# Kernel optimization log

Measured on AMD Instinct MI355X. Metric: run time of the kernel, lower is better.

The kernel has to match this reference:

```python
import jax, jax.numpy as jnp
import numpy as np

L, B, H, E, V = 64, 2048, 1024, 50, 256  # seq_len, batch, hidden, char_emb, char_vocab
PAD = 0


def setup_inputs() -> dict:
    key = jax.random.key(0)
    ks = jax.random.split(key, 10)
    s = 1.0 / np.sqrt(H)  # torch LSTM default init scale
    emb = jax.random.normal(ks[0], (V, E), jnp.float32)
    emb = emb.at[PAD].set(0.0)  # padding_idx row
    return {
        "input": jax.random.randint(ks[1], (L, B), 0, V, jnp.int32),
        "h0": jax.random.normal(ks[2], (1, B, H), jnp.float32),
        "c0": jax.random.normal(ks[3], (1, B, H), jnp.float32),
        "emb": emb,
        "W_ih": jax.random.uniform(ks[4], (4 * H, E), jnp.float32, -s, s),
        "W_hh": jax.random.uniform(ks[5], (4 * H, H), jnp.float32, -s, s),
        "b_ih": jax.random.uniform(ks[6], (4 * H,), jnp.float32, -s, s),
        "b_hh": jax.random.uniform(ks[7], (4 * H,), jnp.float32, -s, s),
        "W_proj": jax.random.uniform(ks[8], (V, H), jnp.float32, -s, s),
        "b_proj": jax.random.uniform(ks[9], (V,), jnp.float32, -s, s),
    }


def reference(input, h0, c0, emb, W_ih, W_hh, b_ih, b_hh, W_proj, b_proj):
    # char embedding lookup: (L, B, E)
    x = emb[input]
    b = b_ih + b_hh

    def step(carry, x_t):
        h, c = carry  # (B, H) each
        gates = x_t @ W_ih.T + h @ W_hh.T + b  # (B, 4H), torch gate order i,f,g,o
        i, f, g, o = jnp.split(gates, 4, axis=-1)
        c_new = jax.nn.sigmoid(f) * c + jax.nn.sigmoid(i) * jnp.tanh(g)
        h_new = jax.nn.sigmoid(o) * jnp.tanh(c_new)
        return (h_new, c_new), h_new

    (hT, cT), hs = jax.lax.scan(step, (h0[0], c0[0]), x)
    # per-step linear projection of hidden state (same math as looped Linear)
    scores = hs @ W_proj.T + b_proj  # (L, B, V)
    return scores, hT[None], cT[None]
```

## Files before the change

kernel.cpp:

```cpp
#include <hip/hip_runtime.h>
#include <hip/hip_bf16.h>
#include <cstdint>
#include <cstddef>

#define LSEQ  64
#define BATCH 2048
#define HID   1024
#define NGATE 4096
#define VOC   256
#define EMBD  50

using bf16 = __hip_bfloat16;
typedef __attribute__((ext_vector_type(8))) __bf16 bf16x8;
typedef __attribute__((ext_vector_type(4))) float  f32x4;

__device__ __forceinline__ void gload_lds16(const void* g, void* l) {
  __builtin_amdgcn_global_load_lds(
      (const __attribute__((address_space(1))) unsigned int*)g,
      (__attribute__((address_space(3))) unsigned int*)l, 16, 0, 0);
}

__device__ __forceinline__ float sigf(float x) {
  x = fminf(fmaxf(x, -30.f), 30.f);
  return 1.f / (1.f + __expf(-x));
}
__device__ __forceinline__ float tanh_f(float x) {
  x = fminf(fmaxf(x, -15.f), 15.f);
  float e = __expf(2.f * x);
  return (e - 1.f) / (e + 1.f);
}


__global__ void k_prep_whh(const float* __restrict__ W, bf16* __restrict__ Wr) {
  size_t i = (size_t)blockIdx.x * 256 + threadIdx.x;
  int k  = (int)(i & 1023);
  int np = (int)(i >> 10);
  int T = np >> 7, w = np & 127;
  int wc = w >> 6, g = (w >> 4) & 3, hl = w & 15;
  int grow = g * HID + T * 32 + wc * 16 + hl;
  Wr[i] = __float2bfloat16(W[(size_t)grow * HID + k]);
}

__global__ void k_prep_embw(const float* __restrict__ emb, const float* __restrict__ W_ih,
                            const float* __restrict__ b_ih, const float* __restrict__ b_hh,
                            float* __restrict__ embW) {
  size_t i = (size_t)blockIdx.x * 256 + threadIdx.x;
  int np = (int)(i & 4095);
  int v  = (int)(i >> 12);
  int T = np >> 7, w = np & 127;
  int wc = w >> 6, g = (w >> 4) & 3, hl = w & 15;
  int grow = g * HID + T * 32 + wc * 16 + hl;
  float s = b_ih[grow] + b_hh[grow];
  #pragma unroll 10
  for (int e = 0; e < EMBD; ++e)
    s += emb[(size_t)v * EMBD + e] * W_ih[(size_t)grow * EMBD + e];
  embW[i] = s;
}

__global__ void k_prep_wp(const float* __restrict__ Wp_f, bf16* __restrict__ Wp) {
  size_t i = (size_t)blockIdx.x * 256 + threadIdx.x;
  Wp[i] = __float2bfloat16(Wp_f[i]);
}

__global__ void k_init_state(const float* __restrict__ h0, const float* __restrict__ c0,
                             bf16* __restrict__ h, float* __restrict__ c) {
  size_t i = (size_t)blockIdx.x * 256 + threadIdx.x;
  h[i] = __float2bfloat16(h0[i]);
  c[i] = c0[i];
}

template<int MODE>
__global__ __launch_bounds__(512) void g8(
    const bf16* __restrict__ Abase, const bf16* __restrict__ Bbase,
    const float* __restrict__ c_in, float* __restrict__ c_out,
    bf16* __restrict__ h_out,
    const float* __restrict__ embW, const int* __restrict__ input,
    const float* __restrict__ b_proj, float* __restrict__ out,
    int t, int kc, int nslots)
{
  __shared__ __align__(16) bf16 lsA[4 * 256 * 32];
  __shared__ __align__(16) bf16 lsB[4 * 128 * 32];

  const int tid  = threadIdx.x;
  const int wave = tid >> 6, lane = tid & 63;
  const int wr = wave >> 1, wc = wave & 1;
  const int bx = blockIdx.x, by = blockIdx.y;

  const bf16* Asrc;
  if constexpr (MODE == 0) {
    Asrc = Abase + (size_t)bx * 256 * HID;
  } else {
    int t_local = bx >> 3;
    int slot = (kc + 1 + t_local) % nslots;
    Asrc = Abase + ((size_t)slot * BATCH + (size_t)(bx & 7) * 256) * HID;
  }
  const bf16* Bsrc = Bbase + (size_t)by * 128 * HID;

  const int srow = tid >> 2;
  const int xg   = (tid >> 3) & 3;
  const int colg = (((tid & 3) ^ xg) << 3);
  const bf16* pA0 = Asrc + (size_t)srow * HID + colg;
  const bf16* pA1 = Asrc + (size_t)(128 + srow) * HID + colg;
  const bf16* pB  = Bsrc + (size_t)srow * HID + colg;
  bf16* dA0 = lsA + wave * 512;
  bf16* dA1 = lsA + 4096 + wave * 512;
  bf16* dB  = lsB + wave * 512;

  const int hl = lane & 15;
  const int kk = (((lane >> 4) ^ ((lane >> 1) & 3)) << 3);
  int aofs[4], bofs[4];
  #pragma unroll
  for (int m = 0; m < 4; ++m) aofs[m] = (wr * 64 + m * 16 + hl) * 32 + kk;
  #pragma unroll
  for (int n = 0; n < 4; ++n) bofs[n] = (wc * 64 + n * 16 + hl) * 32 + kk;

  f32x4 acc[4][4] = {};

#define STAGE(SB_) do {                              \
    gload_lds16(pA0, dA0 + (SB_) * 8192); pA0 += 32; \
    gload_lds16(pA1, dA1 + (SB_) * 8192); pA1 += 32; \
    gload_lds16(pB,  dB  + (SB_) * 4096); pB  += 32; \
  } while (0)

#define TILE(S_, VM_, DOST_) do {                                        \
    asm volatile("s_waitcnt vmcnt(" #VM_ ")" ::: "memory");              \
    __builtin_amdgcn_s_barrier();                                        \
    __builtin_amdgcn_sched_barrier(0);                                   \
    const bf16* aB_ = lsA + (S_) * 8192;                                 \
    const bf16* bB_ = lsB + (S_) * 4096;                                 \
    bf16x8 aF[4], bF[4];                                                 \
    _Pragma("unroll")                                                    \
    for (int m = 0; m < 4; ++m) aF[m] = *(const bf16x8*)(aB_ + aofs[m]); \
    _Pragma("unroll")                                                    \
    for (int n = 0; n < 4; ++n) bF[n] = *(const bf16x8*)(bB_ + bofs[n]); \
    if (DOST_) STAGE(((S_) + 2) & 3);                                    \
    _Pragma("unroll")                                                    \
    for (int m = 0; m < 4; ++m)                                          \
      _Pragma("unroll")                                                  \
      for (int n = 0; n < 4; ++n)                                        \
        acc[m][n] = __builtin_amdgcn_mfma_f32_16x16x32_bf16(aF[m], bF[n], acc[m][n], 0, 0, 0); \
  } while (0)

  STAGE(0);
  STAGE(1);
  for (int kt = 0; kt < 28; kt += 4) {
    TILE(0, 3, 1);
    TILE(1, 3, 1);
    TILE(2, 3, 1);
    TILE(3, 3, 1);
  }
  TILE(0, 3, 1);
  TILE(1, 3, 1);
  TILE(2, 3, 0);
  TILE(3, 0, 0);

#undef STAGE
#undef TILE

  const int qrow = (lane >> 4) * 4;

  if constexpr (MODE == 0) {
    const int h_idx = by * 32 + wc * 16 + hl;
    const float* ewc = embW + (size_t)(by * 128 + wc * 64);
    #pragma unroll
    for (int m = 0; m < 4; ++m) {
      const int b0 = bx * 256 + wr * 64 + m * 16 + qrow;
      const int4 iv = *(const int4*)(input + (size_t)t * BATCH + b0);
      #pragma unroll
      for (int r = 0; r < 4; ++r) {
        const int idx = (&iv.x)[r];
        const float* ew = ewc + (size_t)idx * NGATE;
        float ivv = acc[m][0][r] + ew[hl];
        float fv  = acc[m][1][r] + ew[16 + hl];
        float gv  = acc[m][2][r] + ew[32 + hl];
        float ov  = acc[m][3][r] + ew[48 + hl];
        const size_t off = (size_t)(b0 + r) * HID + h_idx;
        float cn = sigf(fv) * c_in[off] + sigf(ivv) * tanh_f(gv);
        float hn = sigf(ov) * tanh_f(cn);
        h_out[off] = __float2bfloat16(hn);
        c_out[off] = cn;
        if (t == LSEQ - 1) {
          out[(size_t)LSEQ * BATCH * VOC + off] = hn;
          out[(size_t)LSEQ * BATCH * VOC + (size_t)BATCH * HID + off] = cn;
        }
      }
    }
  } else {
    const int t_glob = kc + (bx >> 3);
    float* os = out + (size_t)t_glob * BATCH * VOC;
    const int b0base = (bx & 7) * 256 + wr * 64;
    #pragma unroll
    for (int m = 0; m < 4; ++m) {
      #pragma unroll
      for (int n = 0; n < 4; ++n) {
        const int v = by * 128 + wc * 64 + n * 16 + hl;
        const float bp = b_proj[v];
        #pragma unroll
        for (int r = 0; r < 4; ++r)
          os[(size_t)(b0base + m * 16 + qrow + r) * VOC + v] = acc[m][n][r] + bp;
      }
    }
  }
}


extern "C" void kernel_launch(void* const* d_in, const int* in_sizes, int n_in,
                              void* d_out, int out_size, void* d_ws, size_t ws_size,
                              hipStream_t stream)
{
  (void)in_sizes; (void)n_in; (void)out_size;
  const int*   input  = (const int*)  d_in[0];
  const float* h0     = (const float*)d_in[1];
  const float* c0     = (const float*)d_in[2];
  const float* emb    = (const float*)d_in[3];
  const float* W_ih   = (const float*)d_in[4];
  const float* W_hh   = (const float*)d_in[5];
  const float* b_ih   = (const float*)d_in[6];
  const float* b_hh   = (const float*)d_in[7];
  const float* W_proj = (const float*)d_in[8];
  const float* b_proj = (const float*)d_in[9];
  float* out = (float*)d_out;

  char* ws = (char*)d_ws;
  bf16*  Wr   = (bf16*)(ws);
  bf16*  Wp   = (bf16*)(ws + 8388608);
  float* embW = (float*)(ws + 8912896);
  float* cb0  = (float*)(ws + 13107200);
  float* cb1  = (float*)(ws + 21495808);
  bf16*  hs   = (bf16*)(ws + 29884416);
  const size_t fixed = 29884416;
  const size_t slotB = (size_t)BATCH * HID * sizeof(bf16);

  int nslots = 2;
  const int cand[6] = {65, 17, 9, 5, 3, 2};
  for (int i = 0; i < 6; ++i)
    if (fixed + (size_t)cand[i] * slotB <= ws_size) { nslots = cand[i]; break; }
  const int chunk = nslots - 1;

  k_prep_whh <<<16384, 256, 0, stream>>>(W_hh, Wr);
  k_prep_wp  <<<1024,  256, 0, stream>>>(W_proj, Wp);
  k_prep_embw<<<4096,  256, 0, stream>>>(emb, W_ih, b_ih, b_hh, embW);
  k_init_state<<<8192, 256, 0, stream>>>(h0, c0, hs, cb0);

  float* cbuf[2] = {cb0, cb1};
  for (int kc = 0; kc < LSEQ; kc += chunk) {
    for (int t = kc; t < kc + chunk; ++t) {
      const int si = t % nslots, so = (t + 1) % nslots;
      g8<0><<<dim3(8, 32), 512, 0, stream>>>(
          hs + (size_t)si * BATCH * HID, Wr,
          cbuf[t & 1], cbuf[(t + 1) & 1],
          hs + (size_t)so * BATCH * HID,
          embW, input, b_proj, out, t, 0, 0);
    }
    g8<1><<<dim3(8 * chunk, 2), 512, 0, stream>>>(
        hs, Wp, nullptr, nullptr, nullptr,
        nullptr, nullptr, b_proj, out, 0, kc, nslots);
  }
}
```

Baseline: 2.088 ms.

## Deepen GEMM K-tile to 64, triple-buffer LDS, split phases, remap blocks to XCDs

The inner bf16 MFMA GEMM loop now stages 64-wide K tiles into a 3-slot LDS ring instead of 32-wide tiles in 4 slots. Each tile is computed in two phases, with global-to-LDS loads interleaved and s_setprio raised around the MFMAs. The XOR swizzle is redone for the wider rows. The recurrent-step kernel is launched as a 1D grid whose block ids are remapped so blocks sharing a weight column tile land on the same XCD, aiming for better L2 reuse of W_hh. The goal is fewer barriers per K and better overlap of loads with MFMA, at the cost of more LDS per block and a more fragile wait-count schedule.

```diff
diff --git a/kernel.cpp b/kernel.cpp
--- a/kernel.cpp
+++ b/kernel.cpp
@@ -78,13 +78,22 @@
     const float* __restrict__ b_proj, float* __restrict__ out,
     int t, int kc, int nslots)
 {
-  __shared__ __align__(16) bf16 lsA[4 * 256 * 32];
-  __shared__ __align__(16) bf16 lsB[4 * 128 * 32];
+  __shared__ __align__(16) bf16 lsA[3 * 256 * 64];
+  __shared__ __align__(16) bf16 lsB[3 * 128 * 64];
 
   const int tid  = threadIdx.x;
   const int wave = tid >> 6, lane = tid & 63;
   const int wr = wave >> 1, wc = wave & 1;
-  const int bx = blockIdx.x, by = blockIdx.y;
+  const int hl = lane & 15, q = lane >> 4;
+
+  int bx, by;
+  if constexpr (MODE == 0) {
+    int id = blockIdx.x, xcd = id & 7, idx = id >> 3;
+    by = xcd + ((idx & 3) << 3);
+    bx = idx >> 2;
+  } else {
+    bx = blockIdx.x; by = blockIdx.y;
+  }
 
   const bf16* Asrc;
   if constexpr (MODE == 0) {
@@ -96,68 +105,99 @@
   }
   const bf16* Bsrc = Bbase + (size_t)by * 128 * HID;
 
-  const int srow = tid >> 2;
-  const int xg   = (tid >> 3) & 3;
-  const int colg = (((tid & 3) ^ xg) << 3);
-  const bf16* pA0 = Asrc + (size_t)srow * HID + colg;
-  const bf16* pA1 = Asrc + (size_t)(128 + srow) * HID + colg;
-  const bf16* pB  = Bsrc + (size_t)srow * HID + colg;
-  bf16* dA0 = lsA + wave * 512;
-  bf16* dA1 = lsA + 4096 + wave * 512;
-  bf16* dB  = lsB + wave * 512;
-
-  const int hl = lane & 15;
-  const int kk = (((lane >> 4) ^ ((lane >> 1) & 3)) << 3);
-  int aofs[4], bofs[4];
+  const bf16 *pA0, *pA1, *pA2, *pA3, *pB0, *pB1;
+  {
+    int g0 = tid,      r0 = g0 >> 3, c0v = (g0 & 7) ^ (r0 & 7);
+    int g1 = 512+tid,  r1 = g1 >> 3, c1v = (g1 & 7) ^ (r1 & 7);
+    int g2 = 1024+tid, r2 = g2 >> 3, c2v = (g2 & 7) ^ (r2 & 7);
+    int g3 = 1536+tid, r3 = g3 >> 3, c3v = (g3 & 7) ^ (r3 & 7);
+    pA0 = Asrc + (size_t)r0 * HID + c0v * 8;
+    pA1 = Asrc + (size_t)r1 * HID + c1v * 8;
+    pA2 = Asrc + (size_t)r2 * HID + c2v * 8;
+    pA3 = Asrc + (size_t)r3 * HID + c3v * 8;
+    pB0 = Bsrc + (size_t)r0 * HID + c0v * 8;
+    pB1 = Bsrc + (size_t)r1 * HID + c1v * 8;
+  }
+  bf16* dA = lsA + wave * 512;
+  bf16* dB = lsB + wave * 512;
+
+  int aofs0[4], aofs1[4], bofs0[4], bofs1[4];
   #pragma unroll
-  for (int m = 0; m < 4; ++m) aofs[m] = (wr * 64 + m * 16 + hl) * 32 + kk;
+  for (int m = 0; m < 4; ++m) {
+    int row = wr * 64 + m * 16 + hl;
+    aofs0[m] = row * 64 + ((q ^ (hl & 7)) * 8);
+    aofs1[m] = row * 64 + (((4 + q) ^ (hl & 7)) * 8);
+  }
   #pragma unroll
-  for (int n = 0; n < 4; ++n) bofs[n] = (wc * 64 + n * 16 + hl) * 32 + kk;
+  for (int n = 0; n < 4; ++n) {
+    int row = wc * 64 + n * 16 + hl;
+    bofs0[n] = row * 64 + ((q ^ (hl & 7)) * 8);
+    bofs1[n] = row * 64 + (((4 + q) ^ (hl & 7)) * 8);
+  }
 
   f32x4 acc[4][4] = {};
 
-#define STAGE(SB_) do {                              \
-    gload_lds16(pA0, dA0 + (SB_) * 8192); pA0 += 32; \
-    gload_lds16(pA1, dA1 + (SB_) * 8192); pA1 += 32; \
-    gload_lds16(pB,  dB  + (SB_) * 4096); pB  += 32; \
-  } while (0)
-
-#define TILE(S_, VM_, DOST_) do {                                        \
-    asm volatile("s_waitcnt vmcnt(" #VM_ ")" ::: "memory");              \
-    __builtin_amdgcn_s_barrier();                                        \
-    __builtin_amdgcn_sched_barrier(0);                                   \
-    const bf16* aB_ = lsA + (S_) * 8192;                                 \
-    const bf16* bB_ = lsB + (S_) * 4096;                                 \
-    bf16x8 aF[4], bF[4];                                                 \
-    _Pragma("unroll")                                                    \
-    for (int m = 0; m < 4; ++m) aF[m] = *(const bf16x8*)(aB_ + aofs[m]); \
-    _Pragma("unroll")                                                    \
-    for (int n = 0; n < 4; ++n) bF[n] = *(const bf16x8*)(bB_ + bofs[n]); \
-    if (DOST_) STAGE(((S_) + 2) & 3);                                    \
-    _Pragma("unroll")                                                    \
-    for (int m = 0; m < 4; ++m)                                          \
-      _Pragma("unroll")                                                  \
-      for (int n = 0; n < 4; ++n)                                        \
+#define STG_P0(S_) { gload_lds16(pA0, dA + (S_)*16384);         pA0 += 64;  \
+                     gload_lds16(pA1, dA + (S_)*16384 + 4096);  pA1 += 64;  \
+                     gload_lds16(pA2, dA + (S_)*16384 + 8192);  pA2 += 64; }
+#define STG_P1(S_) { gload_lds16(pA3, dA + (S_)*16384 + 12288); pA3 += 64;  \
+                     gload_lds16(pB0, dB + (S_)*8192);          pB0 += 64;  \
+                     gload_lds16(pB1, dB + (S_)*8192 + 4096);   pB1 += 64; }
+
+#define PHASE(Ab_, Bb_, AO_, BO_, STG_) {                                   \
+    bf16x8 aF[4], bF[4];                                                    \
+    _Pragma("unroll")                                                       \
+    for (int m = 0; m < 4; ++m) aF[m] = *(const bf16x8*)((Ab_) + AO_[m]);   \
+    _Pragma("unroll")                                                       \
+    for (int n = 0; n < 4; ++n) bF[n] = *(const bf16x8*)((Bb_) + BO_[n]);   \
+    STG_;                                                                   \
+    __builtin_amdgcn_s_barrier();                                           \
+    asm volatile("s_waitcnt lgkmcnt(0)" ::: "memory");                      \
+    __builtin_amdgcn_sched_barrier(0);                                      \
+    __builtin_amdgcn_s_setprio(1);                                          \
+    _Pragma("unroll")                                                       \
+    for (int m = 0; m < 4; ++m)                                             \
+      _Pragma("unroll")                                                     \
+      for (int n = 0; n < 4; ++n)                                           \
         acc[m][n] = __builtin_amdgcn_mfma_f32_16x16x32_bf16(aF[m], bF[n], acc[m][n], 0, 0, 0); \
-  } while (0)
-
-  STAGE(0);
-  STAGE(1);
-  for (int kt = 0; kt < 28; kt += 4) {
-    TILE(0, 3, 1);
-    TILE(1, 3, 1);
-    TILE(2, 3, 1);
-    TILE(3, 3, 1);
-  }
-  TILE(0, 3, 1);
-  TILE(1, 3, 1);
-  TILE(2, 3, 0);
-  TILE(3, 0, 0);
-
-#undef STAGE
-#undef TILE
-
-  const int qrow = (lane >> 4) * 4;
+    __builtin_amdgcn_s_setprio(0);                                          \
+  }
+
+  STG_P0(0); STG_P1(0);
+  STG_P0(1); STG_P1(1);
+  __builtin_amdgcn_sched_barrier(0);
+
+  int cur = 0, st = 2;
+  for (int T = 0; T < 15; ++T) {
+    asm volatile("s_waitcnt vmcnt(6)" ::: "memory");
+    __builtin_amdgcn_s_barrier();
+    const bf16* Ab = lsA + cur * 16384;
+    const bf16* Bb = lsB + cur * 8192;
+    if (T < 14) {
+      PHASE(Ab, Bb, aofs0, bofs0, STG_P0(st));
+      PHASE(Ab, Bb, aofs1, bofs1, STG_P1(st));
+    } else {
+      PHASE(Ab, Bb, aofs0, bofs0, );
+      PHASE(Ab, Bb, aofs1, bofs1, );
+    }
+    cur = (cur == 2) ? 0 : cur + 1;
+    st  = (st  == 2) ? 0 : st  + 1;
+  }
+  asm volatile("s_waitcnt vmcnt(0)" ::: "memory");
+  __builtin_amdgcn_s_barrier();
+  {
+    const bf16* Ab = lsA + cur * 16384;
+    const bf16* Bb = lsB + cur * 8192;
+    PHASE(Ab, Bb, aofs0, bofs0, );
+    PHASE(Ab, Bb, aofs1, bofs1, );
+  }
+  __builtin_amdgcn_sched_barrier(0);
+
+#undef STG_P0
+#undef STG_P1
+#undef PHASE
+
+  const int qrow = q * 4;
 
   if constexpr (MODE == 0) {
     const int h_idx = by * 32 + wc * 16 + hl;
@@ -246,7 +286,7 @@
   for (int kc = 0; kc < LSEQ; kc += chunk) {
     for (int t = kc; t < kc + chunk; ++t) {
       const int si = t % nslots, so = (t + 1) % nslots;
-      g8<0><<<dim3(8, 32), 512, 0, stream>>>(
+      g8<0><<<dim3(256), 512, 0, stream>>>(
           hs + (size_t)si * BATCH * HID, Wr,
           cbuf[t & 1], cbuf[(t + 1) & 1],
           hs + (size_t)so * BATCH * HID,
```

Measured after the change: 1.888 ms. 1.11x faster.
